# Kernel optimization log

Hardware: AMD Instinct MI355X
Metric: run time of the kernel (lower is better)

## Reference

```python
import jax, jax.numpy as jnp
import numpy as np

# init_kwargs constants
K = 5                      # kernel_sz
SIGMA_SPATIAL = 2.0
SIGMA_INTENSITY = 0.1
KVAL = -1.0 / (2.0 * SIGMA_SPATIAL ** 2)        # kernel buffer value (same for all k^2 taps)
SIDIV = 1.0 / (2.0 * SIGMA_INTENSITY ** 2)      # sigma_intensity_div


def _extract_block(x, k):
    """F.unfold equivalent: (B,C,H,W) -> (B,H,W,k*k,C), SAME zero padding, row-major taps."""
    B, C, H, W = x.shape
    p = k // 2
    xp = jnp.pad(x, ((0, 0), (0, 0), (p, p), (p, p)))
    # fixed small loop over k*k taps (not a data-dim loop)
    pats = jnp.stack([xp[:, :, i:i + H, j:j + W] for i in range(k) for j in range(k)], axis=2)  # B,C,k2,H,W
    return jnp.transpose(pats, (0, 3, 4, 2, 1))  # B,H,W,k2,C


def setup_inputs() -> dict:
    key = jax.random.key(0)
    k1, k2 = jax.random.split(key)
    template = jax.random.uniform(k1, (1, 3, 1080, 1920), dtype=jnp.float32)
    vector_curr = jax.random.normal(k2, (1, 2, 1080, 1920), dtype=jnp.float32)
    return {"template": template, "vector_curr": vector_curr}


def reference(template, vector_curr):
    # inputs are float32, so cast() is a no-op
    compare_pix = jnp.transpose(template, (0, 2, 3, 1))[:, :, :, None, :]   # B,H,W,1,C
    compare_kernel = _extract_block(template, K)                            # B,H,W,k2,C
    intensity_diff = jnp.sum((compare_pix - compare_kernel) ** 2, axis=-1)  # B,H,W,k2
    coeff = jnp.clip(1.0 - jnp.abs(KVAL - intensity_diff * SIDIV), 0.0, 1.0)[..., None]  # B,H,W,k2,1
    vector_block = _extract_block(vector_curr, K)                           # B,H,W,k2,Cv
    num = jnp.sum(vector_block * coeff, axis=-2)                            # B,H,W,Cv
    den = jnp.sum(coeff, axis=-2)                                           # B,H,W,1
    out = (num / den).astype(jnp.float16)
    return jnp.transpose(out, (0, 3, 1, 2))                                  # B,Cv,H,W fp16
```

## Files before the change

### kernel.cpp

```cpp
#include <hip/hip_runtime.h>


#define IMG_H 1080
#define IMG_W 1920
#define TS_X 64
#define TS_Y 16
#define HALO_H 20
#define HALO_W 72

__global__ __launch_bounds__(256)
void jbf_kernel(const float* __restrict__ tpl,
                const float* __restrict__ vec,
                float* __restrict__ out) {
    constexpr float KVAL  = -0.125f;
    constexpr float SIDIV = 50.0f;

    __shared__ __align__(16) float smem[5][HALO_H][HALO_W];

    const int tid = threadIdx.x;
    const int x0  = blockIdx.x * TS_X;
    const int y0  = blockIdx.y * TS_Y;

#pragma unroll
    for (int c = 0; c < 5; ++c) {
        const float* __restrict__ src =
            (c < 3) ? (tpl + c * (IMG_H * IMG_W)) : (vec + (c - 3) * (IMG_H * IMG_W));
        for (int i = tid; i < HALO_H * HALO_W; i += 256) {
            const int r   = i / HALO_W;
            const int col = i - r * HALO_W;
            const int gy  = y0 + r - 2;
            const int gx  = x0 + col - 2;
            float v = 0.0f;
            if (gy >= 0 && gy < IMG_H && gx >= 0 && gx < IMG_W)
                v = src[gy * IMG_W + gx];
            smem[c][r][col] = v;
        }
    }
    __syncthreads();

    const int tx = tid & 15;
    const int ty = tid >> 4;
    const int lx = tx * 4;

    float num0[4] = {0.f, 0.f, 0.f, 0.f};
    float num1[4] = {0.f, 0.f, 0.f, 0.f};
    float den [4] = {0.f, 0.f, 0.f, 0.f};

    float c0[4], c1[4], c2[4];
#pragma unroll
    for (int px = 0; px < 4; ++px) {
        c0[px] = smem[0][ty + 2][lx + 2 + px];
        c1[px] = smem[1][ty + 2][lx + 2 + px];
        c2[px] = smem[2][ty + 2][lx + 2 + px];
    }

#pragma unroll
    for (int dy = 0; dy < 5; ++dy) {
        const int row = ty + dy;
        float4 a0 = *(const float4*)&smem[0][row][lx];
        float4 b0 = *(const float4*)&smem[0][row][lx + 4];
        float4 a1 = *(const float4*)&smem[1][row][lx];
        float4 b1 = *(const float4*)&smem[1][row][lx + 4];
        float4 a2 = *(const float4*)&smem[2][row][lx];
        float4 b2 = *(const float4*)&smem[2][row][lx + 4];
        float4 av0 = *(const float4*)&smem[3][row][lx];
        float4 bv0 = *(const float4*)&smem[3][row][lx + 4];
        float4 av1 = *(const float4*)&smem[4][row][lx];
        float4 bv1 = *(const float4*)&smem[4][row][lx + 4];

        const float w0[8]  = {a0.x, a0.y, a0.z, a0.w, b0.x, b0.y, b0.z, b0.w};
        const float w1[8]  = {a1.x, a1.y, a1.z, a1.w, b1.x, b1.y, b1.z, b1.w};
        const float w2[8]  = {a2.x, a2.y, a2.z, a2.w, b2.x, b2.y, b2.z, b2.w};
        const float wv0[8] = {av0.x, av0.y, av0.z, av0.w, bv0.x, bv0.y, bv0.z, bv0.w};
        const float wv1[8] = {av1.x, av1.y, av1.z, av1.w, bv1.x, bv1.y, bv1.z, bv1.w};

#pragma unroll
        for (int dx = 0; dx < 5; ++dx) {
#pragma unroll
            for (int px = 0; px < 4; ++px) {
                const int k = dx + px;
                const float d0 = c0[px] - w0[k];
                const float d1 = c1[px] - w1[k];
                const float d2 = c2[px] - w2[k];
                const float id = d0 * d0 + d1 * d1 + d2 * d2;
                const float t  = fabsf(KVAL - id * SIDIV);
                float coeff = 1.0f - t;
                coeff = fminf(fmaxf(coeff, 0.0f), 1.0f);
                num0[px] += wv0[k] * coeff;
                num1[px] += wv1[k] * coeff;
                den [px] += coeff;
            }
        }
    }

    const int gy = y0 + ty;
    if (gy < IMG_H) {
        const int gx = x0 + lx;
        float4 o0, o1;
        float r0 = __builtin_amdgcn_rcpf(den[0]);
        float r1 = __builtin_amdgcn_rcpf(den[1]);
        float r2 = __builtin_amdgcn_rcpf(den[2]);
        float r3 = __builtin_amdgcn_rcpf(den[3]);
        o0.x = num0[0] * r0; o0.y = num0[1] * r1; o0.z = num0[2] * r2; o0.w = num0[3] * r3;
        o1.x = num1[0] * r0; o1.y = num1[1] * r1; o1.z = num1[2] * r2; o1.w = num1[3] * r3;
        *(float4*)(out + (size_t)0 * IMG_H * IMG_W + gy * IMG_W + gx) = o0;
        *(float4*)(out + (size_t)1 * IMG_H * IMG_W + gy * IMG_W + gx) = o1;
    }
}

extern "C" void kernel_launch(void* const* d_in, const int* in_sizes, int n_in,
                              void* d_out, int out_size, void* d_ws, size_t ws_size,
                              hipStream_t stream) {
    const float* tpl = (const float*)d_in[0];
    const float* vec = (const float*)d_in[1];
    float* out = (float*)d_out;

    dim3 grid(IMG_W / TS_X, (IMG_H + TS_Y - 1) / TS_Y);
    jbf_kernel<<<grid, 256, 0, stream>>>(tpl, vec, out);
}
```

Measured before the change: 135.0 us.

## Replace shared-memory tiling with register-streamed rows and expanded distance algebra

The kernel drops the shared-memory halo tile. Each 64-thread block now streams input rows straight from global memory into double-buffered registers and keeps five rolling output-row accumulators. The squared distance is expanded as |c|^2 + |t|^2 - 2c·t, so per-tap norms are shared across outputs, and the abs/clip is folded into a single fmax, assuming the value never exceeds 1. This removes LDS traffic and the block-wide barrier and reduces ALU work per tap. In exchange it uses more registers, has only one wave per block, and the expanded form can lose precision through cancellation.

```diff
diff --git a/kernel.cpp b/kernel.cpp
--- a/kernel.cpp
+++ b/kernel.cpp
@@ -3,108 +3,154 @@
 
 #define IMG_H 1080
 #define IMG_W 1920
-#define TS_X 64
-#define TS_Y 16
-#define HALO_H 20
-#define HALO_W 72
+#define IMG_HW (IMG_H * IMG_W)
 
-__global__ __launch_bounds__(256)
+typedef float f4u __attribute__((ext_vector_type(4), aligned(4)));
+typedef float f2u __attribute__((ext_vector_type(2), aligned(8)));
+
+__global__ __launch_bounds__(64)
 void jbf_kernel(const float* __restrict__ tpl,
                 const float* __restrict__ vec,
-                float* __restrict__ out) {
-    constexpr float KVAL  = -0.125f;
-    constexpr float SIDIV = 50.0f;
+                float* __restrict__ out)
+{
+    const int lane = threadIdx.x;
+    const int bx = blockIdx.x, by = blockIdx.y;
+    const int x0  = bx * 128;
+    const int gy0 = by * 8;
+    const int x   = x0 + 2 * lane;
+    const bool hborder = (bx == 0) | (bx == 14);
 
-    __shared__ __align__(16) float smem[5][HALO_H][HALO_W];
+    float m[6];
+    int   co[6];
+#pragma unroll
+    for (int j = 0; j < 6; ++j) {
+        const int c = x - 2 + j;
+        m[j]  = (c >= 0 && c < IMG_W) ? 1.0f : 0.0f;
+        co[j] = c < 0 ? 0 : (c >= IMG_W ? IMG_W - 1 : c);
+    }
 
-    const int tid = threadIdx.x;
-    const int x0  = blockIdx.x * TS_X;
-    const int y0  = blockIdx.y * TS_Y;
+    const float* chp[5] = { tpl, tpl + IMG_HW, tpl + 2 * IMG_HW, vec, vec + IMG_HW };
+
+    float sc[5][3][2];
+    float sA[5][2];
+    float n0[5][2], n1[5][2], dn[5][2];
+#pragma unroll
+    for (int s = 0; s < 5; ++s)
+#pragma unroll
+        for (int p = 0; p < 2; ++p) {
+            sc[s][0][p] = 0.f; sc[s][1][p] = 0.f; sc[s][2][p] = 0.f;
+            sA[s][p] = 0.875f; n0[s][p] = 0.f; n1[s][p] = 0.f; dn[s][p] = 0.f;
+        }
+
+    float tb[2][5][6];
+    float cb[3][2];
+
+    auto row_clamp = [](int gr) { return gr < 0 ? 0 : (gr >= IMG_H ? IMG_H - 1 : gr); };
+
+    auto load_tap = [&](int b, int gr) {
+        const int rb = row_clamp(gr) * IMG_W;
+        if (!hborder) {
+#pragma unroll
+            for (int c = 0; c < 5; ++c) {
+                const float* p = chp[c] + rb + (x - 2);
+                const f4u a = *(const f4u*)p;
+                const f2u q = *(const f2u*)(p + 4);
+                tb[b][c][0] = a.x; tb[b][c][1] = a.y; tb[b][c][2] = a.z;
+                tb[b][c][3] = a.w; tb[b][c][4] = q.x; tb[b][c][5] = q.y;
+            }
+        } else {
+#pragma unroll
+            for (int c = 0; c < 5; ++c)
+#pragma unroll
+                for (int j = 0; j < 6; ++j)
+                    tb[b][c][j] = chp[c][rb + co[j]];
+        }
+    };
+
+    auto load_cen = [&](int gr) {
+        const int rb = row_clamp(gr) * IMG_W;
+#pragma unroll
+        for (int c = 0; c < 3; ++c) {
+            const f2u v = *(const f2u*)(chp[c] + rb + x);
+            cb[c][0] = v.x; cb[c][1] = v.y;
+        }
+    };
+
+    auto mask_row = [&](int b, bool rowvalid) {
+        if (!rowvalid) {
+#pragma unroll
+            for (int c = 0; c < 5; ++c)
+#pragma unroll
+                for (int j = 0; j < 6; ++j) tb[b][c][j] = 0.0f;
+        } else if (hborder) {
+#pragma unroll
+            for (int c = 0; c < 5; ++c)
+#pragma unroll
+                for (int j = 0; j < 6; ++j) tb[b][c][j] *= m[j];
+        }
+    };
+
+    auto activate = [&](int s) {
+#pragma unroll
+        for (int p = 0; p < 2; ++p) {
+            const float c0 = cb[0][p], c1 = cb[1][p], c2 = cb[2][p];
+            sc[s][0][p] = c0; sc[s][1][p] = c1; sc[s][2][p] = c2;
+            const float S = c0 * c0 + c1 * c1 + c2 * c2;
+            sA[s][p] = __builtin_fmaf(S, -50.0f, 0.875f);
+            n0[s][p] = 0.f; n1[s][p] = 0.f; dn[s][p] = 0.f;
+        }
+    };
+
+    auto taps = [&](int b) {
+        float T[6];
+#pragma unroll
+        for (int k = 0; k < 6; ++k)
+            T[k] = tb[b][0][k] * tb[b][0][k] + tb[b][1][k] * tb[b][1][k]
+                 + tb[b][2][k] * tb[b][2][k];
+#pragma unroll
+        for (int s = 0; s < 5; ++s)
+#pragma unroll
+            for (int dx = 0; dx < 5; ++dx)
+#pragma unroll
+                for (int p = 0; p < 2; ++p) {
+                    const int k = dx + p;
+                    const float dot = sc[s][0][p] * tb[b][0][k]
+                                    + sc[s][1][p] * tb[b][1][k]
+                                    + sc[s][2][p] * tb[b][2][k];
+                    const float B = __builtin_fmaf(T[k], -50.0f, sA[s][p]);
+                    const float coeff = fmaxf(__builtin_fmaf(dot, 100.0f, B), 0.0f);
+                    n0[s][p] = __builtin_fmaf(tb[b][3][k], coeff, n0[s][p]);
+                    n1[s][p] = __builtin_fmaf(tb[b][4][k], coeff, n1[s][p]);
+                    dn[s][p] += coeff;
+                }
+    };
+
+    auto retire = [&](int s, int y) {
+        const float r0 = __builtin_amdgcn_rcpf(dn[s][0]);
+        const float r1 = __builtin_amdgcn_rcpf(dn[s][1]);
+        f2u o0, o1;
+        o0.x = n0[s][0] * r0; o0.y = n0[s][1] * r1;
+        o1.x = n1[s][0] * r0; o1.y = n1[s][1] * r1;
+        *(f2u*)(out + (size_t)y * IMG_W + x) = o0;
+        *(f2u*)(out + IMG_HW + (size_t)y * IMG_W + x) = o1;
+    };
+
+    load_tap(0, gy0 - 2);
+    load_cen(gy0);
 
 #pragma unroll
-    for (int c = 0; c < 5; ++c) {
-        const float* __restrict__ src =
-            (c < 3) ? (tpl + c * (IMG_H * IMG_W)) : (vec + (c - 3) * (IMG_H * IMG_W));
-        for (int i = tid; i < HALO_H * HALO_W; i += 256) {
-            const int r   = i / HALO_W;
-            const int col = i - r * HALO_W;
-            const int gy  = y0 + r - 2;
-            const int gx  = x0 + col - 2;
-            float v = 0.0f;
-            if (gy >= 0 && gy < IMG_H && gx >= 0 && gx < IMG_W)
-                v = src[gy * IMG_W + gx];
-            smem[c][r][col] = v;
+    for (int r = 0; r < 12; ++r) {
+        const int b  = r & 1;
+        const int gr = gy0 - 2 + r;
+        if (r < 11) load_tap(1 - b, gr + 1);
+        if (r < 8) {
+            activate((r + 4) % 5);
+            if (r < 7) load_cen(gy0 + r + 1);
         }
-    }
-    __syncthreads();
-
-    const int tx = tid & 15;
-    const int ty = tid >> 4;
-    const int lx = tx * 4;
-
-    float num0[4] = {0.f, 0.f, 0.f, 0.f};
-    float num1[4] = {0.f, 0.f, 0.f, 0.f};
-    float den [4] = {0.f, 0.f, 0.f, 0.f};
-
-    float c0[4], c1[4], c2[4];
-#pragma unroll
-    for (int px = 0; px < 4; ++px) {
-        c0[px] = smem[0][ty + 2][lx + 2 + px];
-        c1[px] = smem[1][ty + 2][lx + 2 + px];
-        c2[px] = smem[2][ty + 2][lx + 2 + px];
-    }
-
-#pragma unroll
-    for (int dy = 0; dy < 5; ++dy) {
-        const int row = ty + dy;
-        float4 a0 = *(const float4*)&smem[0][row][lx];
-        float4 b0 = *(const float4*)&smem[0][row][lx + 4];
-        float4 a1 = *(const float4*)&smem[1][row][lx];
-        float4 b1 = *(const float4*)&smem[1][row][lx + 4];
-        float4 a2 = *(const float4*)&smem[2][row][lx];
-        float4 b2 = *(const float4*)&smem[2][row][lx + 4];
-        float4 av0 = *(const float4*)&smem[3][row][lx];
-        float4 bv0 = *(const float4*)&smem[3][row][lx + 4];
-        float4 av1 = *(const float4*)&smem[4][row][lx];
-        float4 bv1 = *(const float4*)&smem[4][row][lx + 4];
-
-        const float w0[8]  = {a0.x, a0.y, a0.z, a0.w, b0.x, b0.y, b0.z, b0.w};
-        const float w1[8]  = {a1.x, a1.y, a1.z, a1.w, b1.x, b1.y, b1.z, b1.w};
-        const float w2[8]  = {a2.x, a2.y, a2.z, a2.w, b2.x, b2.y, b2.z, b2.w};
-        const float wv0[8] = {av0.x, av0.y, av0.z, av0.w, bv0.x, bv0.y, bv0.z, bv0.w};
-        const float wv1[8] = {av1.x, av1.y, av1.z, av1.w, bv1.x, bv1.y, bv1.z, bv1.w};
-
-#pragma unroll
-        for (int dx = 0; dx < 5; ++dx) {
-#pragma unroll
-            for (int px = 0; px < 4; ++px) {
-                const int k = dx + px;
-                const float d0 = c0[px] - w0[k];
-                const float d1 = c1[px] - w1[k];
-                const float d2 = c2[px] - w2[k];
-                const float id = d0 * d0 + d1 * d1 + d2 * d2;
-                const float t  = fabsf(KVAL - id * SIDIV);
-                float coeff = 1.0f - t;
-                coeff = fminf(fmaxf(coeff, 0.0f), 1.0f);
-                num0[px] += wv0[k] * coeff;
-                num1[px] += wv1[k] * coeff;
-                den [px] += coeff;
-            }
-        }
-    }
-
-    const int gy = y0 + ty;
-    if (gy < IMG_H) {
-        const int gx = x0 + lx;
-        float4 o0, o1;
-        float r0 = __builtin_amdgcn_rcpf(den[0]);
-        float r1 = __builtin_amdgcn_rcpf(den[1]);
-        float r2 = __builtin_amdgcn_rcpf(den[2]);
-        float r3 = __builtin_amdgcn_rcpf(den[3]);
-        o0.x = num0[0] * r0; o0.y = num0[1] * r1; o0.z = num0[2] * r2; o0.w = num0[3] * r3;
-        o1.x = num1[0] * r0; o1.y = num1[1] * r1; o1.z = num1[2] * r2; o1.w = num1[3] * r3;
-        *(float4*)(out + (size_t)0 * IMG_H * IMG_W + gy * IMG_W + gx) = o0;
-        *(float4*)(out + (size_t)1 * IMG_H * IMG_W + gy * IMG_W + gx) = o1;
+        const bool rowvalid = (gr >= 0) & (gr < IMG_H);
+        mask_row(b, rowvalid);
+        taps(b);
+        if (r >= 4) retire(r % 5, gy0 + r - 4);
     }
 }
 
@@ -115,6 +161,6 @@
     const float* vec = (const float*)d_in[1];
     float* out = (float*)d_out;
 
-    dim3 grid(IMG_W / TS_X, (IMG_H + TS_Y - 1) / TS_Y);
-    jbf_kernel<<<grid, 256, 0, stream>>>(tpl, vec, out);
+    dim3 grid(IMG_W / 128, IMG_H / 8);
+    jbf_kernel<<<grid, 64, 0, stream>>>(tpl, vec, out);
 }
```

After: 117.7 us. 1.15x faster.
